# Optimization experiments

Measured on AMD Instinct MI355X. Metric: run time of the kernel, lower is better.

## Reference

```python
import math
import jax, jax.numpy as jnp
import numpy as np

B, S, D_MODEL = 4, 2048, 1024
N_HEADS, D_KV = 16, 64
INNER = N_HEADS * D_KV
NUM_BUCKETS = 32
MAX_DISTANCE = 128


def _relative_position_bucket(relative_position, bidirectional=True,
                              num_buckets=32, max_distance=128):
    # Faithful port of T5Attention._relative_position_bucket
    ret = jnp.zeros_like(relative_position)
    n = -relative_position
    if bidirectional:
        num_buckets //= 2
        ret = ret + (n < 0).astype(jnp.int32) * num_buckets
        n = jnp.abs(n)
    else:
        n = jnp.maximum(n, 0)
    max_exact = num_buckets // 2
    is_small = n < max_exact
    # safe log: n>=max_exact wherever this branch is selected
    val_if_large = max_exact + (
        jnp.log(jnp.maximum(n, 1).astype(jnp.float32) / max_exact)
        / math.log(max_distance / max_exact) * (num_buckets - max_exact)
    ).astype(jnp.int32)
    val_if_large = jnp.minimum(val_if_large, num_buckets - 1)
    return ret + jnp.where(is_small, n, val_if_large)


def setup_inputs() -> dict:
    key = jax.random.key(0)
    k_h, k_q, k_k, k_v, k_o, k_e = jax.random.split(key, 6)
    std = D_MODEL ** -0.5
    return {
        "hidden_states": jax.random.normal(k_h, (B, S, D_MODEL), dtype=jnp.float32),
        "Wq": jax.random.normal(k_q, (D_MODEL, INNER), dtype=jnp.float32) * std,
        "Wk": jax.random.normal(k_k, (D_MODEL, INNER), dtype=jnp.float32) * std,
        "Wv": jax.random.normal(k_v, (D_MODEL, INNER), dtype=jnp.float32) * std,
        "Wo": jax.random.normal(k_o, (INNER, D_MODEL), dtype=jnp.float32) * std,
        "rel_emb": jax.random.normal(k_e, (NUM_BUCKETS, N_HEADS), dtype=jnp.float32) * std,
    }


def reference(hidden_states, Wq, Wk, Wv, Wo, rel_emb):
    b, s, _ = hidden_states.shape
    # QKV projections (T5: no bias, no 1/sqrt(d) scaling of scores)
    def shape_heads(x):  # [b, s, inner] -> [b, h, s, d_kv]
        return x.reshape(b, s, N_HEADS, D_KV).transpose(0, 2, 1, 3)
    q = shape_heads(hidden_states @ Wq)
    k = shape_heads(hidden_states @ Wk)
    v = shape_heads(hidden_states @ Wv)

    scores = jnp.einsum("bhqd,bhkd->bhqk", q, k)  # [b, h, s, s]

    # relative position bias: sequential_relative_position + bucket + embed
    context_pos = jnp.arange(s, dtype=jnp.int32)[:, None]
    memory_pos = jnp.arange(s, dtype=jnp.int32)[None, :]
    rel_pos = memory_pos - context_pos  # [s, s]
    rp_bucket = _relative_position_bucket(rel_pos, bidirectional=True,
                                          num_buckets=NUM_BUCKETS,
                                          max_distance=MAX_DISTANCE)
    bias = rel_emb[rp_bucket]                       # [s, s, h]
    bias = bias.transpose(2, 0, 1)[None]            # [1, h, s, s]

    weights = jax.nn.softmax(scores + bias, axis=-1)
    context = jnp.einsum("bhqk,bhkd->bhqd", weights, v)
    context = context.transpose(0, 2, 1, 3).reshape(b, s, INNER)
    return context @ Wo
```

## Files before the change

### kernel.cpp

```cpp
#include <hip/hip_runtime.h>

typedef __bf16 bf16_t;
typedef __bf16 bf16x4 __attribute__((ext_vector_type(4)));
typedef __bf16 bf16x8 __attribute__((ext_vector_type(8)));
typedef float f32x4 __attribute__((ext_vector_type(4)));

#define NB 4
#define SS 2048
#define DM 1024
#define NH 16
#define DK 64
#define MM (NB*SS)
#define LOG2E 1.44269504f

__global__ __launch_bounds__(256) void k_convert(const float* __restrict__ in,
                                                 bf16_t* __restrict__ out, int n4) {
  int i = blockIdx.x * 256 + threadIdx.x;
  if (i < n4) {
    float4 v = ((const float4*)in)[i];
    bf16x4 o = {(bf16_t)v.x, (bf16_t)v.y, (bf16_t)v.z, (bf16_t)v.w};
    *(bf16x4*)(out + 4 * (size_t)i) = o;
  }
}

__global__ __launch_bounds__(256) void k_transpose(
    const float* __restrict__ W0, const float* __restrict__ W1,
    const float* __restrict__ W2, const float* __restrict__ W3,
    bf16_t* __restrict__ T0, bf16_t* __restrict__ T1,
    bf16_t* __restrict__ T2, bf16_t* __restrict__ T3) {
  __shared__ float t[64][65];
  const float* W = blockIdx.z == 0 ? W0 : blockIdx.z == 1 ? W1 : blockIdx.z == 2 ? W2 : W3;
  bf16_t* T = blockIdx.z == 0 ? T0 : blockIdx.z == 1 ? T1 : blockIdx.z == 2 ? T2 : T3;
  int k0 = blockIdx.y * 64, n0 = blockIdx.x * 64;
  int tid = threadIdx.x;
#pragma unroll
  for (int i = 0; i < 16; i++) {
    int idx = tid + i * 256; int r = idx >> 6, c = idx & 63;
    t[r][c] = W[(size_t)(k0 + r) * DM + n0 + c];
  }
  __syncthreads();
#pragma unroll
  for (int i = 0; i < 16; i++) {
    int idx = tid + i * 256; int r = idx >> 6, c = idx & 63;
    T[(size_t)(n0 + r) * DM + k0 + c] = (bf16_t)t[c][r];
  }
}

__global__ __launch_bounds__(256) void k_bias(const float* __restrict__ rel_emb,
                                              float* __restrict__ biasT) {
  int t = blockIdx.x * 256 + threadIdx.x;
  if (t >= 2 * SS - 1) return;
  int rel = t - (SS - 1);
  int n = -rel;
  int ret = 0;
  if (n < 0) { ret = 16; n = -n; }
  int bucket;
  if (n < 8) bucket = n;
  else {
    int v = 8 + (int)(logf((float)n * 0.125f) * (8.0f / logf(16.0f)));
    bucket = v < 15 ? v : 15;
  }
  bucket += ret;
#pragma unroll
  for (int h = 0; h < NH; h++)
    biasT[h * (2 * SS - 1) + t] = rel_emb[bucket * NH + h] * LOG2E;
}

__device__ __forceinline__ void gld16(const bf16_t* g, bf16_t* l) {
  __builtin_amdgcn_global_load_lds(
      (const __attribute__((address_space(1))) unsigned int*)g,
      (__attribute__((address_space(3))) unsigned int*)l, 16, 0, 0);
}

__device__ __forceinline__ void gemm_tile(const bf16_t* __restrict__ A,
                                          const bf16_t* __restrict__ Bt, const int K,
                                          const int m0, const int n0,
                                          bf16_t* As, bf16_t* Bs, f32x4 (&acc)[4][4]) {
  const int tid = threadIdx.x;
  const int lane = tid & 63, wave = tid >> 6;
  const int l15 = lane & 15, quad = lane >> 4;
  const int wm = (wave >> 1) * 64, wn = (wave & 1) * 64;
  const int wwu = __builtin_amdgcn_readfirstlane(wave);
  const f32x4 z4 = {0.f, 0.f, 0.f, 0.f};
#pragma unroll
  for (int i = 0; i < 4; i++)
#pragma unroll
    for (int j = 0; j < 4; j++) acc[i][j] = z4;

  const int rr = lane >> 2;
  const int cc = (lane & 3) * 8;
  for (int k0 = 0; k0 < K; k0 += 32) {
    __syncthreads();
    gld16(A + (size_t)(m0 + wwu * 32 + rr) * K + k0 + cc,       As + wwu * 1024);
    gld16(A + (size_t)(m0 + wwu * 32 + 16 + rr) * K + k0 + cc,  As + wwu * 1024 + 512);
    gld16(Bt + (size_t)(n0 + wwu * 32 + rr) * K + k0 + cc,      Bs + wwu * 1024);
    gld16(Bt + (size_t)(n0 + wwu * 32 + 16 + rr) * K + k0 + cc, Bs + wwu * 1024 + 512);
    __syncthreads();
    bf16x8 af[4], bfr[4];
#pragma unroll
    for (int i = 0; i < 4; i++) {
      af[i]  = *(const bf16x8*)(As + (wm + i * 16 + l15) * 32 + quad * 8);
      bfr[i] = *(const bf16x8*)(Bs + (wn + i * 16 + l15) * 32 + quad * 8);
    }
#pragma unroll
    for (int i = 0; i < 4; i++)
#pragma unroll
      for (int j = 0; j < 4; j++)
        acc[i][j] = __builtin_amdgcn_mfma_f32_16x16x32_bf16(af[i], bfr[j], acc[i][j], 0, 0, 0);
  }
}

__global__ __launch_bounds__(256) void k_gemm_qkv(
    const bf16_t* __restrict__ A, const bf16_t* __restrict__ Wqt,
    const bf16_t* __restrict__ Wkt, const bf16_t* __restrict__ Wvt,
    bf16_t* __restrict__ Q, bf16_t* __restrict__ Ko, bf16_t* __restrict__ Vt) {
  __shared__ bf16_t As[128 * 32];
  __shared__ bf16_t Bs[128 * 32];
  const int which = blockIdx.z;
  const bf16_t* Bt = which == 0 ? Wqt : (which == 1 ? Wkt : Wvt);
  const int m0 = blockIdx.y * 128, n0 = blockIdx.x * 128;
  f32x4 acc[4][4];
  gemm_tile(A, Bt, DM, m0, n0, As, Bs, acc);

  const int tid = threadIdx.x;
  const int lane = tid & 63, wave = tid >> 6;
  const int l15 = lane & 15, quad = lane >> 4;
  const int wm = (wave >> 1) * 64, wn = (wave & 1) * 64;

  if (which < 2) {
    bf16_t* dst = which == 0 ? Q : Ko;
    const float qs = which == 0 ? LOG2E : 1.0f;
#pragma unroll
    for (int i = 0; i < 4; i++)
#pragma unroll
      for (int j = 0; j < 4; j++)
#pragma unroll
        for (int r = 0; r < 4; r++) {
          int m = m0 + wm + i * 16 + quad * 4 + r;
          int n = n0 + wn + j * 16 + l15;
          int b = m >> 11, s = m & (SS - 1);
          int h = n >> 6, d = n & 63;
          dst[(((size_t)(b * NH + h)) * SS + s) * DK + d] = (bf16_t)(acc[i][j][r] * qs);
        }
  } else {
#pragma unroll
    for (int i = 0; i < 4; i++)
#pragma unroll
      for (int j = 0; j < 4; j++) {
        int m = m0 + wm + i * 16 + quad * 4;
        int n = n0 + wn + j * 16 + l15;
        int b = m >> 11, s = m & (SS - 1);
        int h = n >> 6, d = n & 63;
        int p = s >> 5, off = s & 31;
        bf16x4 pk = {(bf16_t)acc[i][j][0], (bf16_t)acc[i][j][1],
                     (bf16_t)acc[i][j][2], (bf16_t)acc[i][j][3]};
        *(bf16x4*)(&Vt[(((size_t)((b * NH + h) * 64 + p)) * DK + d) * 32 + off]) = pk;
      }
  }
}

__global__ __launch_bounds__(256, 2) void k_attn(const bf16_t* __restrict__ Qg,
                                                 const bf16_t* __restrict__ Kg,
                                                 const bf16_t* __restrict__ Vt,
                                                 const float* __restrict__ biasT,
                                                 bf16_t* __restrict__ ctx) {
  const int bh = blockIdx.y;
  const int b = bh >> 4, h = bh & 15;
  const int it0 = blockIdx.x * 128;
  const bf16_t* Qp = Qg + ((size_t)bh * SS + it0) * DK;
  const bf16_t* Kp = Kg + (size_t)bh * SS * DK;
  const bf16_t* VtP = Vt + (size_t)bh * 64 * DK * 32;
  const float* biasH = biasT + h * (2 * SS - 1);

  __shared__ bf16_t KV[2][2][8][512];
  __shared__ float bias2a[2175][2];
  __shared__ float OsumS[2][4][16];

  const int tid = threadIdx.x;
  const int lane = tid & 63, wave = tid >> 6;
  const int l15 = lane & 15, quad = lane >> 4;
  const int kh = wave & 1, qh = wave >> 1;
  const int kperm = 8 * (l15 >> 2) + (l15 & 3);

  for (int u = tid; u < 2175; u += 256) {
    int g0 = u - it0 + 1920;
    int g1 = g0 + 1;
    g0 = g0 < 0 ? 0 : (g0 > 2 * SS - 2 ? 2 * SS - 2 : g0);
    g1 = g1 < 0 ? 0 : (g1 > 2 * SS - 2 ? 2 * SS - 2 : g1);
    bias2a[u][0] = biasH[g0];
    bias2a[u][1] = biasH[g1];
  }

  auto stage = [&](int buf, int j0) {
    {
      int t = wave;
      const bf16_t* g = Kp + (size_t)(j0 + 32 * (t >> 1) + 4 * (t & 1) + kperm) * DK + quad * 8;
      gld16(g,      &KV[buf][0][t * 2 + 0][0]);
      gld16(g + 32, &KV[buf][0][t * 2 + 1][0]);
    }
    {
      int c = wave >> 1, nib = (wave & 1) * 2;
      const bf16_t* g = VtP + ((size_t)((j0 >> 5) + c) * DK + nib * 16 + l15) * 32 + quad * 8;
      gld16(g,           &KV[buf][1][c * 4 + nib][0]);
      gld16(g + 16 * 32, &KV[buf][1][c * 4 + nib + 1][0]);
    }
  };

  bf16x8 qf[4][2];
#pragma unroll
  for (int mi = 0; mi < 4; mi++) {
    const bf16_t* qr = Qp + (size_t)(64 * qh + mi * 16 + l15) * DK + quad * 8;
    qf[mi][0] = *(const bf16x8*)qr;
    qf[mi][1] = *(const bf16x8*)(qr + 32);
  }

  f32x4 accO[4][4], accS[4];
  const f32x4 z4 = {0.f, 0.f, 0.f, 0.f};
#pragma unroll
  for (int mi = 0; mi < 4; mi++) {
    accS[mi] = z4;
#pragma unroll
    for (int ni = 0; ni < 4; ni++) accO[mi][ni] = z4;
  }
  const bf16_t one = (bf16_t)1.0f;
  const bf16x8 ones = {one, one, one, one, one, one, one, one};

  stage(0, 0);
  const int ub0 = 32 * kh - 64 * qh + 8 * quad - l15 + 127;

  for (int it = 0; it < 32; ++it) {
    const int cb = it & 1;
    __syncthreads();
    if (it < 31) stage(cb ^ 1, (it + 1) * 64);

    bf16x8 kf[2][2], vf[4];
#pragma unroll
    for (int t = 0; t < 2; t++)
#pragma unroll
      for (int hf = 0; hf < 2; hf++)
        kf[t][hf] = *(const bf16x8*)&KV[cb][0][(2 * kh + t) * 2 + hf][lane * 8];
#pragma unroll
    for (int ni = 0; ni < 4; ni++)
      vf[ni] = *(const bf16x8*)&KV[cb][1][kh * 4 + ni][lane * 8];

    const int jb = it * 64 + ub0;
#pragma unroll
    for (int mi = 0; mi < 4; mi++) {
      const int ub = jb - mi * 16;
      float2 a0 = *(const float2*)bias2a[ub],     b0 = *(const float2*)bias2a[ub + 2];
      float2 a1 = *(const float2*)bias2a[ub + 4], b1 = *(const float2*)bias2a[ub + 6];
      f32x4 c0 = {a0.x, a0.y, b0.x, b0.y};
      f32x4 c1 = {a1.x, a1.y, b1.x, b1.y};
      f32x4 s0 = __builtin_amdgcn_mfma_f32_16x16x32_bf16(
          kf[0][1], qf[mi][1],
          __builtin_amdgcn_mfma_f32_16x16x32_bf16(kf[0][0], qf[mi][0], c0, 0, 0, 0), 0, 0, 0);
      f32x4 s1 = __builtin_amdgcn_mfma_f32_16x16x32_bf16(
          kf[1][1], qf[mi][1],
          __builtin_amdgcn_mfma_f32_16x16x32_bf16(kf[1][0], qf[mi][0], c1, 0, 0, 0), 0, 0, 0);
      bf16x8 pf = {(bf16_t)exp2f(s0[0]), (bf16_t)exp2f(s0[1]),
                   (bf16_t)exp2f(s0[2]), (bf16_t)exp2f(s0[3]),
                   (bf16_t)exp2f(s1[0]), (bf16_t)exp2f(s1[1]),
                   (bf16_t)exp2f(s1[2]), (bf16_t)exp2f(s1[3])};
#pragma unroll
      for (int ni = 0; ni < 4; ni++)
        accO[mi][ni] = __builtin_amdgcn_mfma_f32_16x16x32_bf16(vf[ni], pf, accO[mi][ni], 0, 0, 0);
      accS[mi] = __builtin_amdgcn_mfma_f32_16x16x32_bf16(ones, pf, accS[mi], 0, 0, 0);
    }
  }

  __syncthreads();
  f32x4* Ored = (f32x4*)&KV[0][0][0][0];
  if (kh) {
#pragma unroll
    for (int mi = 0; mi < 4; mi++) {
#pragma unroll
      for (int ni = 0; ni < 4; ni++)
        Ored[((qh * 4 + mi) * 4 + ni) * 64 + lane] = accO[mi][ni];
      if (quad == 0) OsumS[qh][mi][l15] = accS[mi][0];
    }
  }
  __syncthreads();
  if (!kh) {
#pragma unroll
    for (int mi = 0; mi < 4; mi++) {
      float l = accS[mi][0] + OsumS[qh][mi][l15];
      float inv = 1.0f / l;
      int srow = it0 + 64 * qh + mi * 16 + l15;
#pragma unroll
      for (int ni = 0; ni < 4; ni++) {
        f32x4 o = accO[mi][ni] + Ored[((qh * 4 + mi) * 4 + ni) * 64 + lane];
        bf16x4 pk = {(bf16_t)(o[0] * inv), (bf16_t)(o[1] * inv),
                     (bf16_t)(o[2] * inv), (bf16_t)(o[3] * inv)};
        *(bf16x4*)(&ctx[((size_t)(b * SS + srow)) * DM + h * DK + ni * 16 + quad * 4]) = pk;
      }
    }
  }
}

__global__ __launch_bounds__(256) void k_gemm_out(const bf16_t* __restrict__ A,
                                                  const bf16_t* __restrict__ Wot,
                                                  float* __restrict__ out) {
  __shared__ bf16_t As[128 * 32];
  __shared__ bf16_t Bs[128 * 32];
  const int m0 = blockIdx.y * 128, n0 = blockIdx.x * 128;
  f32x4 acc[4][4];
  gemm_tile(A, Wot, DM, m0, n0, As, Bs, acc);

  const int tid = threadIdx.x;
  const int lane = tid & 63, wave = tid >> 6;
  const int l15 = lane & 15, quad = lane >> 4;
  const int wm = (wave >> 1) * 64, wn = (wave & 1) * 64;
#pragma unroll
  for (int i = 0; i < 4; i++)
#pragma unroll
    for (int j = 0; j < 4; j++)
#pragma unroll
      for (int r = 0; r < 4; r++) {
        int m = m0 + wm + i * 16 + quad * 4 + r;
        int n = n0 + wn + j * 16 + l15;
        out[(size_t)m * DM + n] = acc[i][j][r];
      }
}

extern "C" void kernel_launch(void* const* d_in, const int* in_sizes, int n_in,
                              void* d_out, int out_size, void* d_ws, size_t ws_size,
                              hipStream_t stream) {
  (void)in_sizes; (void)n_in; (void)out_size; (void)ws_size;
  const float* H  = (const float*)d_in[0];
  const float* Wq = (const float*)d_in[1];
  const float* Wk = (const float*)d_in[2];
  const float* Wv = (const float*)d_in[3];
  const float* Wo = (const float*)d_in[4];
  const float* rel = (const float*)d_in[5];
  float* out = (float*)d_out;

  char* w = (char*)d_ws;
  bf16_t* Hbf = (bf16_t*)w; w += (size_t)MM * DM * 2;
  bf16_t* Wqt = (bf16_t*)w; w += (size_t)DM * DM * 2;
  bf16_t* Wkt = (bf16_t*)w; w += (size_t)DM * DM * 2;
  bf16_t* Wvt = (bf16_t*)w; w += (size_t)DM * DM * 2;
  bf16_t* Wot = (bf16_t*)w; w += (size_t)DM * DM * 2;
  bf16_t* Q   = (bf16_t*)w; w += (size_t)MM * DM * 2;
  bf16_t* K   = (bf16_t*)w; w += (size_t)MM * DM * 2;
  bf16_t* Vt  = (bf16_t*)w; w += (size_t)MM * DM * 2;
  bf16_t* CTX = (bf16_t*)w; w += (size_t)MM * DM * 2;
  float* biasT = (float*)w;

  k_convert<<<MM * DM / 4 / 256, 256, 0, stream>>>(H, Hbf, MM * DM / 4);
  k_transpose<<<dim3(16, 16, 4), 256, 0, stream>>>(Wq, Wk, Wv, Wo, Wqt, Wkt, Wvt, Wot);
  k_bias<<<(2 * SS - 1 + 255) / 256, 256, 0, stream>>>(rel, biasT);
  k_gemm_qkv<<<dim3(DM / 128, MM / 128, 3), 256, 0, stream>>>(Hbf, Wqt, Wkt, Wvt, Q, K, Vt);
  k_attn<<<dim3(SS / 128, NB * NH), 256, 0, stream>>>(Q, K, Vt, biasT, CTX);
  k_gemm_out<<<dim3(DM / 128, MM / 128), 256, 0, stream>>>(CTX, Wot, out);
}
```

Before: 312.2 us.

## Shrink bias LDS table to a band with constant tails, raise attention occupancy

The relative-position bias table in shared memory shrinks from 2175 pairs to a 512-entry band around the diagonal. Key tiles outside the band use a single splatted constant, since buckets saturate at large distances. This cuts LDS use and the prologue fill loop, and launch bounds now request 4 blocks per SM instead of 2. exp2f is replaced with the raw hardware exp2 intrinsic to drop range handling. The higher occupancy target may force register spilling given the large accumulator arrays, and correctness depends on the band limits matching the bucket saturation distance.

```diff
diff --git a/kernel.cpp b/kernel.cpp
--- a/kernel.cpp
+++ b/kernel.cpp
@@ -159,7 +159,7 @@
   }
 }
 
-__global__ __launch_bounds__(256, 2) void k_attn(const bf16_t* __restrict__ Qg,
+__global__ __launch_bounds__(256, 4) void k_attn(const bf16_t* __restrict__ Qg,
                                                  const bf16_t* __restrict__ Kg,
                                                  const bf16_t* __restrict__ Vt,
                                                  const float* __restrict__ biasT,
@@ -173,7 +173,7 @@
   const float* biasH = biasT + h * (2 * SS - 1);
 
   __shared__ bf16_t KV[2][2][8][512];
-  __shared__ float bias2a[2175][2];
+  __shared__ float bias2[512][2];
   __shared__ float OsumS[2][4][16];
 
   const int tid = threadIdx.x;
@@ -182,14 +182,13 @@
   const int kh = wave & 1, qh = wave >> 1;
   const int kperm = 8 * (l15 >> 2) + (l15 & 3);
 
-  for (int u = tid; u < 2175; u += 256) {
-    int g0 = u - it0 + 1920;
-    int g1 = g0 + 1;
-    g0 = g0 < 0 ? 0 : (g0 > 2 * SS - 2 ? 2 * SS - 2 : g0);
-    g1 = g1 < 0 ? 0 : (g1 > 2 * SS - 2 ? 2 * SS - 2 : g1);
-    bias2a[u][0] = biasH[g0];
-    bias2a[u][1] = biasH[g1];
-  }
+  for (int w = tid; w < 512; w += 256) {
+    int g = w - 256 + (SS - 1);
+    bias2[w][0] = biasH[g];
+    bias2[w][1] = biasH[g + 1];
+  }
+  const float Bpos = biasH[(SS - 1) + 1024];
+  const float Bneg = biasH[(SS - 1) - 1024];
 
   auto stage = [&](int buf, int j0) {
     {
@@ -226,7 +225,7 @@
   const bf16x8 ones = {one, one, one, one, one, one, one, one};
 
   stage(0, 0);
-  const int ub0 = 32 * kh - 64 * qh + 8 * quad - l15 + 127;
+  const int wb0 = 32 * kh + 8 * quad - 64 * qh - l15 - it0 + 256;
 
   for (int it = 0; it < 32; ++it) {
     const int cb = it & 1;
@@ -243,24 +242,35 @@
     for (int ni = 0; ni < 4; ni++)
       vf[ni] = *(const bf16x8*)&KV[cb][1][kh * 4 + ni][lane * 8];
 
-    const int jb = it * 64 + ub0;
+    const int diff = it * 64 - it0;
+    const bool band = (diff >= -128) && (diff < 256);
+    const float cconst = diff >= 256 ? Bpos : Bneg;
+    const f32x4 csplat = {cconst, cconst, cconst, cconst};
+    const int jb = it * 64 + wb0;
+
 #pragma unroll
     for (int mi = 0; mi < 4; mi++) {
-      const int ub = jb - mi * 16;
-      float2 a0 = *(const float2*)bias2a[ub],     b0 = *(const float2*)bias2a[ub + 2];
-      float2 a1 = *(const float2*)bias2a[ub + 4], b1 = *(const float2*)bias2a[ub + 6];
-      f32x4 c0 = {a0.x, a0.y, b0.x, b0.y};
-      f32x4 c1 = {a1.x, a1.y, b1.x, b1.y};
+      f32x4 c0, c1;
+      if (band) {
+        const int w = jb - mi * 16;
+        float2 a0 = *(const float2*)bias2[w],     b0 = *(const float2*)bias2[w + 2];
+        float2 a1 = *(const float2*)bias2[w + 4], b1 = *(const float2*)bias2[w + 6];
+        c0 = f32x4{a0.x, a0.y, b0.x, b0.y};
+        c1 = f32x4{a1.x, a1.y, b1.x, b1.y};
+      } else {
+        c0 = csplat;
+        c1 = csplat;
+      }
       f32x4 s0 = __builtin_amdgcn_mfma_f32_16x16x32_bf16(
           kf[0][1], qf[mi][1],
           __builtin_amdgcn_mfma_f32_16x16x32_bf16(kf[0][0], qf[mi][0], c0, 0, 0, 0), 0, 0, 0);
       f32x4 s1 = __builtin_amdgcn_mfma_f32_16x16x32_bf16(
           kf[1][1], qf[mi][1],
           __builtin_amdgcn_mfma_f32_16x16x32_bf16(kf[1][0], qf[mi][0], c1, 0, 0, 0), 0, 0, 0);
-      bf16x8 pf = {(bf16_t)exp2f(s0[0]), (bf16_t)exp2f(s0[1]),
-                   (bf16_t)exp2f(s0[2]), (bf16_t)exp2f(s0[3]),
-                   (bf16_t)exp2f(s1[0]), (bf16_t)exp2f(s1[1]),
-                   (bf16_t)exp2f(s1[2]), (bf16_t)exp2f(s1[3])};
+      bf16x8 pf = {(bf16_t)__builtin_amdgcn_exp2f(s0[0]), (bf16_t)__builtin_amdgcn_exp2f(s0[1]),
+                   (bf16_t)__builtin_amdgcn_exp2f(s0[2]), (bf16_t)__builtin_amdgcn_exp2f(s0[3]),
+                   (bf16_t)__builtin_amdgcn_exp2f(s1[0]), (bf16_t)__builtin_amdgcn_exp2f(s1[1]),
+                   (bf16_t)__builtin_amdgcn_exp2f(s1[2]), (bf16_t)__builtin_amdgcn_exp2f(s1[3])};
 #pragma unroll
       for (int ni = 0; ni < 4; ni++)
         accO[mi][ni] = __builtin_amdgcn_mfma_f32_16x16x32_bf16(vf[ni], pf, accO[mi][ni], 0, 0, 0);
```

Result: slower. 607.0 us (+94.5%).
